# Optimization experiments

Hardware: AMD Instinct MI355X
Metric: run time of the kernel (lower is better)

## Reference

```python
import jax, jax.numpy as jnp
import numpy as np
from jax import lax

WEIGHT = 1.0
NUM_DILATION_STEPS = 20
FAR_DIST = 20.0


def _neighbor_count(x, kernel, num_classes):
    # grouped 3x3 conv with center tap zeroed, SAME padding (stride 1)
    return lax.conv_general_dilated(
        x, kernel, window_strides=(1, 1), padding='SAME',
        feature_group_count=num_classes,
        dimension_numbers=('NCHW', 'OIHW', 'NCHW'))


def fast_sdf(target_mask, num_classes):
    # target_mask: [B, H, W] int labels -> per-class chamfer-ish distance map [B, C, H, W]
    one_hot = jnp.transpose(jax.nn.one_hot(target_mask, num_classes, dtype=jnp.float32),
                            (0, 3, 1, 2))  # [B, C, H, W]
    foreground = (one_hot > 0.5).astype(jnp.float32)

    # 3x3 all-ones kernel with center zero, one per class (grouped conv)
    k = np.ones((num_classes, 1, 3, 3), dtype=np.float32)
    k[:, 0, 1, 1] = 0.0
    kernel = jnp.asarray(k)

    dist_map0 = jnp.zeros_like(foreground)

    def step(i, state):
        dist_map, current_mask = state
        dilated = (_neighbor_count(current_mask, kernel, num_classes) > 0).astype(jnp.float32)
        # note: faithful to torch code -- pixels with no neighbors vanish and
        # contribute negative increments, exactly as `dilated - current_mask` does
        new_pixels = dilated - current_mask
        dist_map = dist_map + new_pixels * (i + 1).astype(jnp.float32)
        return (dist_map, dilated)

    dist_map, current_mask = lax.fori_loop(0, NUM_DILATION_STEPS, step,
                                           (dist_map0, foreground))
    return jnp.where(current_mask == 0, FAR_DIST, dist_map)


def setup_inputs() -> dict:
    key = jax.random.key(0)
    k1, k2 = jax.random.split(key)
    B, C, H, W = 8, 19, 512, 512
    pred = jax.random.normal(k1, (B, C, H, W), dtype=jnp.float32)
    target = jax.random.randint(k2, (B, H, W), 0, C, dtype=jnp.int64)
    return {"pred": pred, "target": target}


def reference(pred, target):
    num_classes = pred.shape[1]
    probs = jax.nn.softmax(pred, axis=1)
    gt_sdf = lax.stop_gradient(fast_sdf(target, num_classes))
    loss = jnp.mean(probs * gt_sdf)
    return WEIGHT * loss
```

## Files before the change

kernel.cpp:

```cpp
#include <hip/hip_runtime.h>

#define B_ 8
#define C_ 19
#define H_ 512
#define W_ 512
#define HW_ (H_*W_)

#define HALO   20
#define INTR   8
#define WIN    48
#define NSTRIP 64

typedef unsigned long long u64;

__global__ __launch_bounds__(256) void mask_kernel(const int* __restrict__ target,
                                                   u64* __restrict__ masks) {
    __shared__ u64 mlds[64][21];
    const int blk  = blockIdx.x;
    const int b    = blk >> 6;
    const int base = (blk & 63) * 64;
    const int tid  = threadIdx.x;
    const int lane = tid & 63, wv = tid >> 6;
    const int* tgt = target + b * HW_;
    for (int t = 0; t < 16; ++t) {
        const int cl = wv * 16 + t;
        const int x  = tgt[(base + cl) * 64 + lane];
        u64 keep = 0;
        #pragma unroll
        for (int c = 0; c < C_; ++c) {
            u64 m = __ballot(x == c);
            if (lane == c) keep = m;
        }
        if (lane < C_) mlds[cl][lane] = keep;
    }
    __syncthreads();
    for (int idx = tid; idx < C_ * 64; idx += 256) {
        const int c = idx >> 6, wl = idx & 63;
        masks[((size_t)b * C_ + c) * 4096 + base + wl] = mlds[wl][c];
    }
}

__global__ __launch_bounds__(256, 2) void fused_kernel(const u64* __restrict__ masks,
                                                       const float* __restrict__ pred,
                                                       float* __restrict__ out) {
    __shared__ unsigned char sdfl[C_ * INTR * W_];
    __shared__ float part[4];
    const int blk   = blockIdx.x;
    const int strip = blk & 63;
    const int b     = blk >> 6;
    const int tid   = threadIdx.x;
    const int wv    = tid >> 6, lane = tid & 63;
    const int w     = lane & 7, g = lane >> 3;
    const int gytop = strip * INTR - HALO;

    for (int c = wv; c < C_; c += 4) {
        const u64* mk = masks + ((size_t)b * C_ + c) * 4096;
        u64 cov[6], h[6], iso[6], pl[6][5];

        #pragma unroll
        for (int i = 0; i < 6; ++i) {
            const int gy = gytop + g * 6 + i;
            cov[i] = (gy >= 0 && gy < H_) ? mk[gy * 8 + w] : 0;
            iso[i] = 0;
            #pragma unroll
            for (int j = 0; j < 5; ++j) pl[i][j] = 0;
        }

        u64 nc[6];
        {
            unsigned mp = 0, lp = 0;
            #pragma unroll
            for (int i = 0; i < 6; ++i) {
                mp |= (unsigned)(cov[i] >> 63) << i;
                lp |= ((unsigned)cov[i] & 1) << i;
            }
            unsigned fl = __shfl_up(mp, 1);   if (w == 0) fl = 0;
            unsigned fr = __shfl_down(lp, 1); if (w == 7) fr = 0;
            #pragma unroll
            for (int i = 0; i < 6; ++i) {
                nc[i] = (cov[i] << 1) | (cov[i] >> 1) | (u64)((fl >> i) & 1) | ((u64)((fr >> i) & 1) << 63);
                h[i]  = nc[i] | cov[i];
            }
        }

        bool active;
        {
            u64 hup = __shfl_up(h[5], 8);   if (g == 0) hup = 0;
            u64 hdn = __shfl_down(h[0], 8); if (g == 7) hdn = 0;
            u64 d[6], diffw = 0;
            #pragma unroll
            for (int i = 0; i < 6; ++i) {
                const u64 up  = (i > 0) ? h[i - 1] : hup;
                const u64 dn  = (i < 5) ? h[i + 1] : hdn;
                const u64 nbr = nc[i] | up | dn;
                iso[i] = cov[i] & ~nbr;
                const u64 nb = nbr & ~cov[i];
                pl[i][0] = nb;
                d[i] = cov[i] | nbr;
                diffw |= nb;
                cov[i] = d[i];
            }
            unsigned mp = 0, lp = 0;
            #pragma unroll
            for (int i = 0; i < 6; ++i) {
                mp |= (unsigned)(cov[i] >> 63) << i;
                lp |= ((unsigned)cov[i] & 1) << i;
            }
            unsigned fl = __shfl_up(mp, 1);   if (w == 0) fl = 0;
            unsigned fr = __shfl_down(lp, 1); if (w == 7) fr = 0;
            #pragma unroll
            for (int i = 0; i < 6; ++i)
                h[i] = cov[i] | (cov[i] << 1) | (cov[i] >> 1) | (u64)((fl >> i) & 1) | ((u64)((fr >> i) & 1) << 63);
            active = __any(diffw != 0);
        }

        if (active) {
            #pragma unroll
            for (int s = 2; s <= 19; ++s) {
                u64 hup = __shfl_up(h[5], 8);   if (g == 0) hup = 0;
                u64 hdn = __shfl_down(h[0], 8); if (g == 7) hdn = 0;
                u64 diffw = 0;
                #pragma unroll
                for (int i = 0; i < 6; ++i) {
                    const u64 up = (i > 0) ? h[i - 1] : hup;
                    const u64 dn = (i < 5) ? h[i + 1] : hdn;
                    const u64 d  = up | h[i] | dn;
                    const u64 nb = d ^ cov[i];
                    diffw |= nb;
                    if (s & 1)  pl[i][0] |= nb;
                    if (s & 2)  pl[i][1] |= nb;
                    if (s & 4)  pl[i][2] |= nb;
                    if (s & 8)  pl[i][3] |= nb;
                    if (s & 16) pl[i][4] |= nb;
                    cov[i] = d;
                }
                if (!__any(diffw != 0)) break;
                if (s < 19) {
                    unsigned mp = 0, lp = 0;
                    #pragma unroll
                    for (int i = 0; i < 6; ++i) {
                        mp |= (unsigned)(cov[i] >> 63) << i;
                        lp |= ((unsigned)cov[i] & 1) << i;
                    }
                    unsigned fl = __shfl_up(mp, 1);   if (w == 0) fl = 0;
                    unsigned fr = __shfl_down(lp, 1); if (w == 7) fr = 0;
                    #pragma unroll
                    for (int i = 0; i < 6; ++i)
                        h[i] = cov[i] | (cov[i] << 1) | (cov[i] >> 1) | (u64)((fl >> i) & 1) | ((u64)((fr >> i) & 1) << 63);
                }
            }
        }

        #pragma unroll
        for (int i = 0; i < 6; ++i) {
            const int lr = g * 6 + i;
            if (lr < HALO || lr >= HALO + INTR) continue;
            pl[i][0] |= iso[i];
            const u64 m = ~cov[i];
            pl[i][2] |= m;
            pl[i][4] |= m;
            u64* dst = (u64*)&sdfl[(c * INTR + (lr - HALO)) * W_ + w * 64];
            #pragma unroll
            for (int g2 = 0; g2 < 8; ++g2) {
                u64 x = 0;
                #pragma unroll
                for (int j = 0; j < 5; ++j)
                    x |= ((pl[i][j] >> (8 * g2)) & 0xFFULL) << (8 * j);
                u64 t;
                t = (x ^ (x >> 7))  & 0x00AA00AA00AA00AAULL; x ^= t ^ (t << 7);
                t = (x ^ (x >> 14)) & 0x0000CCCC0000CCCCULL; x ^= t ^ (t << 14);
                t = (x ^ (x >> 28)) & 0x00000000F0F0F0F0ULL; x ^= t ^ (t << 28);
                dst[g2] = x;
            }
        }
    }
    __syncthreads();

    float acc = 0.f;
    const float* pb = pred + (size_t)b * C_ * HW_ + (size_t)strip * INTR * W_;
    #pragma unroll
    for (int k = 0; k < 4; ++k) {
        const int p = k * 1024 + tid * 4;
        float4 den = {0.f, 0.f, 0.f, 0.f};
        float4 num = {0.f, 0.f, 0.f, 0.f};
        #pragma unroll
        for (int c = 0; c < C_; ++c) {
            const float4 v  = *(const float4*)(pb + (size_t)c * HW_ + p);
            const uchar4 sv = *(const uchar4*)&sdfl[c * 4096 + p];
            const float e0 = __expf(v.x), e1 = __expf(v.y);
            const float e2 = __expf(v.z), e3 = __expf(v.w);
            den.x += e0; den.y += e1; den.z += e2; den.w += e3;
            num.x = fmaf(e0, (float)sv.x, num.x);
            num.y = fmaf(e1, (float)sv.y, num.y);
            num.z = fmaf(e2, (float)sv.z, num.z);
            num.w = fmaf(e3, (float)sv.w, num.w);
        }
        acc += num.x / den.x + num.y / den.y + num.z / den.z + num.w / den.w;
    }

    #pragma unroll
    for (int off = 32; off > 0; off >>= 1) acc += __shfl_down(acc, off);
    if ((tid & 63) == 0) part[tid >> 6] = acc;
    __syncthreads();
    if (tid == 0) {
        float s = (part[0] + part[1]) + (part[2] + part[3]);
        atomicAdd(out, s * (1.0f / 39845888.0f));
    }
}

extern "C" void kernel_launch(void* const* d_in, const int* in_sizes, int n_in,
                              void* d_out, int out_size, void* d_ws, size_t ws_size,
                              hipStream_t stream) {
    const float* pred   = (const float*)d_in[0];
    const int*   target = (const int*)d_in[1];
    u64* masks = (u64*)d_ws;
    float* out = (float*)d_out;

    hipMemsetAsync(out, 0, sizeof(float), stream);
    mask_kernel<<<512, 256, 0, stream>>>(target, masks);
    fused_kernel<<<B_ * NSTRIP, 256, 0, stream>>>(masks, pred, out);
}
```

Baseline: 279.9 us.

## Split fused dilation+loss into separate dilate and loss kernels via workspace SDF

Splits the fused kernel in two. A dilate kernel runs one class per wave across five class-groups, which gives five times as many blocks and uses a much smaller LDS buffer, and writes a byte SDF map to global workspace. A separate streaming loss kernel then reads pred and the SDF to compute the softmax-weighted sum. This is meant to raise occupancy and parallelism, since the old fused kernel had only 512 blocks and used about 78KB of LDS. In exchange it adds about 40MB of global SDF writes and reads plus an extra launch, and the old path is kept as a fallback when the workspace is too small.

```diff
diff --git a/kernel.cpp b/kernel.cpp
--- a/kernel.cpp
+++ b/kernel.cpp
@@ -10,8 +10,12 @@
 #define INTR   8
 #define WIN    48
 #define NSTRIP 64
+#define CG_    5
 
 typedef unsigned long long u64;
+
+#define MASKS_BYTES 4980736ULL
+#define SDF_BYTES   39845888ULL
 
 __global__ __launch_bounds__(256) void mask_kernel(const int* __restrict__ target,
                                                    u64* __restrict__ masks) {
@@ -40,20 +44,21 @@
     }
 }
 
-__global__ __launch_bounds__(256, 2) void fused_kernel(const u64* __restrict__ masks,
-                                                       const float* __restrict__ pred,
-                                                       float* __restrict__ out) {
-    __shared__ unsigned char sdfl[C_ * INTR * W_];
-    __shared__ float part[4];
+__global__ __launch_bounds__(256) void dilate_kernel(const u64* __restrict__ masks,
+                                                     unsigned char* __restrict__ sdf) {
+    __shared__ unsigned char sdfl[4 * INTR * W_];
     const int blk   = blockIdx.x;
-    const int strip = blk & 63;
-    const int b     = blk >> 6;
+    const int cg    = blk % CG_;
+    const int rem   = blk / CG_;
+    const int strip = rem & 63;
+    const int b     = rem >> 6;
     const int tid   = threadIdx.x;
     const int wv    = tid >> 6, lane = tid & 63;
     const int w     = lane & 7, g = lane >> 3;
     const int gytop = strip * INTR - HALO;
-
-    for (int c = wv; c < C_; c += 4) {
+    const int c     = cg * 4 + wv;
+
+    if (c < C_) {
         const u64* mk = masks + ((size_t)b * C_ + c) * 4096;
         u64 cov[6], h[6], iso[6], pl[6][5];
 
@@ -159,7 +164,7 @@
             const u64 m = ~cov[i];
             pl[i][2] |= m;
             pl[i][4] |= m;
-            u64* dst = (u64*)&sdfl[(c * INTR + (lr - HALO)) * W_ + w * 64];
+            u64* dst = (u64*)&sdfl[(wv * INTR + (lr - HALO)) * W_ + w * 64];
             #pragma unroll
             for (int g2 = 0; g2 < 8; ++g2) {
                 u64 x = 0;
@@ -176,6 +181,187 @@
     }
     __syncthreads();
 
+    for (int idx = tid; idx < 4 * INTR * W_ / 16; idx += 256) {
+        const int cc = idx >> 8;
+        const int cl = cg * 4 + cc;
+        if (cl >= C_) continue;
+        const int off = (idx & 255) << 4;
+        *(uint4*)(sdf + ((size_t)b * C_ + cl) * HW_ + (size_t)strip * INTR * W_ + off) =
+            *(const uint4*)(&sdfl[cc * (INTR * W_) + off]);
+    }
+}
+
+__global__ __launch_bounds__(256) void loss_kernel(const float* __restrict__ pred,
+                                                   const unsigned char* __restrict__ sdf,
+                                                   float* __restrict__ out) {
+    __shared__ float part[4];
+    const int tid = threadIdx.x;
+    const size_t q = (size_t)blockIdx.x * 256 + tid;
+    const int b = (int)(q >> 16);
+    const int p = ((int)q & 65535) << 2;
+    const float* pb = pred + (size_t)b * C_ * HW_ + p;
+    const unsigned char* sb = sdf + (size_t)b * C_ * HW_ + p;
+    float4 den = {0.f, 0.f, 0.f, 0.f};
+    float4 num = {0.f, 0.f, 0.f, 0.f};
+    #pragma unroll
+    for (int c = 0; c < C_; ++c) {
+        const float4 v  = *(const float4*)(pb + (size_t)c * HW_);
+        const uchar4 sv = *(const uchar4*)(sb + (size_t)c * HW_);
+        const float e0 = __expf(v.x), e1 = __expf(v.y);
+        const float e2 = __expf(v.z), e3 = __expf(v.w);
+        den.x += e0; den.y += e1; den.z += e2; den.w += e3;
+        num.x = fmaf(e0, (float)sv.x, num.x);
+        num.y = fmaf(e1, (float)sv.y, num.y);
+        num.z = fmaf(e2, (float)sv.z, num.z);
+        num.w = fmaf(e3, (float)sv.w, num.w);
+    }
+    float acc = num.x / den.x + num.y / den.y + num.z / den.z + num.w / den.w;
+    #pragma unroll
+    for (int off = 32; off > 0; off >>= 1) acc += __shfl_down(acc, off);
+    if ((tid & 63) == 0) part[tid >> 6] = acc;
+    __syncthreads();
+    if (tid == 0) {
+        float s = (part[0] + part[1]) + (part[2] + part[3]);
+        atomicAdd(out, s * (1.0f / 39845888.0f));
+    }
+}
+
+__global__ __launch_bounds__(256, 2) void fused_kernel(const u64* __restrict__ masks,
+                                                       const float* __restrict__ pred,
+                                                       float* __restrict__ out) {
+    __shared__ unsigned char sdfl[C_ * INTR * W_];
+    __shared__ float part[4];
+    const int blk   = blockIdx.x;
+    const int strip = blk & 63;
+    const int b     = blk >> 6;
+    const int tid   = threadIdx.x;
+    const int wv    = tid >> 6, lane = tid & 63;
+    const int w     = lane & 7, g = lane >> 3;
+    const int gytop = strip * INTR - HALO;
+
+    for (int c = wv; c < C_; c += 4) {
+        const u64* mk = masks + ((size_t)b * C_ + c) * 4096;
+        u64 cov[6], h[6], iso[6], pl[6][5];
+
+        #pragma unroll
+        for (int i = 0; i < 6; ++i) {
+            const int gy = gytop + g * 6 + i;
+            cov[i] = (gy >= 0 && gy < H_) ? mk[gy * 8 + w] : 0;
+            iso[i] = 0;
+            #pragma unroll
+            for (int j = 0; j < 5; ++j) pl[i][j] = 0;
+        }
+
+        u64 nc[6];
+        {
+            unsigned mp = 0, lp = 0;
+            #pragma unroll
+            for (int i = 0; i < 6; ++i) {
+                mp |= (unsigned)(cov[i] >> 63) << i;
+                lp |= ((unsigned)cov[i] & 1) << i;
+            }
+            unsigned fl = __shfl_up(mp, 1);   if (w == 0) fl = 0;
+            unsigned fr = __shfl_down(lp, 1); if (w == 7) fr = 0;
+            #pragma unroll
+            for (int i = 0; i < 6; ++i) {
+                nc[i] = (cov[i] << 1) | (cov[i] >> 1) | (u64)((fl >> i) & 1) | ((u64)((fr >> i) & 1) << 63);
+                h[i]  = nc[i] | cov[i];
+            }
+        }
+
+        bool active;
+        {
+            u64 hup = __shfl_up(h[5], 8);   if (g == 0) hup = 0;
+            u64 hdn = __shfl_down(h[0], 8); if (g == 7) hdn = 0;
+            u64 d[6], diffw = 0;
+            #pragma unroll
+            for (int i = 0; i < 6; ++i) {
+                const u64 up  = (i > 0) ? h[i - 1] : hup;
+                const u64 dn  = (i < 5) ? h[i + 1] : hdn;
+                const u64 nbr = nc[i] | up | dn;
+                iso[i] = cov[i] & ~nbr;
+                const u64 nb = nbr & ~cov[i];
+                pl[i][0] = nb;
+                d[i] = cov[i] | nbr;
+                diffw |= nb;
+                cov[i] = d[i];
+            }
+            unsigned mp = 0, lp = 0;
+            #pragma unroll
+            for (int i = 0; i < 6; ++i) {
+                mp |= (unsigned)(cov[i] >> 63) << i;
+                lp |= ((unsigned)cov[i] & 1) << i;
+            }
+            unsigned fl = __shfl_up(mp, 1);   if (w == 0) fl = 0;
+            unsigned fr = __shfl_down(lp, 1); if (w == 7) fr = 0;
+            #pragma unroll
+            for (int i = 0; i < 6; ++i)
+                h[i] = cov[i] | (cov[i] << 1) | (cov[i] >> 1) | (u64)((fl >> i) & 1) | ((u64)((fr >> i) & 1) << 63);
+            active = __any(diffw != 0);
+        }
+
+        if (active) {
+            #pragma unroll
+            for (int s = 2; s <= 19; ++s) {
+                u64 hup = __shfl_up(h[5], 8);   if (g == 0) hup = 0;
+                u64 hdn = __shfl_down(h[0], 8); if (g == 7) hdn = 0;
+                u64 diffw = 0;
+                #pragma unroll
+                for (int i = 0; i < 6; ++i) {
+                    const u64 up = (i > 0) ? h[i - 1] : hup;
+                    const u64 dn = (i < 5) ? h[i + 1] : hdn;
+                    const u64 d  = up | h[i] | dn;
+                    const u64 nb = d ^ cov[i];
+                    diffw |= nb;
+                    if (s & 1)  pl[i][0] |= nb;
+                    if (s & 2)  pl[i][1] |= nb;
+                    if (s & 4)  pl[i][2] |= nb;
+                    if (s & 8)  pl[i][3] |= nb;
+                    if (s & 16) pl[i][4] |= nb;
+                    cov[i] = d;
+                }
+                if (!__any(diffw != 0)) break;
+                if (s < 19) {
+                    unsigned mp = 0, lp = 0;
+                    #pragma unroll
+                    for (int i = 0; i < 6; ++i) {
+                        mp |= (unsigned)(cov[i] >> 63) << i;
+                        lp |= ((unsigned)cov[i] & 1) << i;
+                    }
+                    unsigned fl = __shfl_up(mp, 1);   if (w == 0) fl = 0;
+                    unsigned fr = __shfl_down(lp, 1); if (w == 7) fr = 0;
+                    #pragma unroll
+                    for (int i = 0; i < 6; ++i)
+                        h[i] = cov[i] | (cov[i] << 1) | (cov[i] >> 1) | (u64)((fl >> i) & 1) | ((u64)((fr >> i) & 1) << 63);
+                }
+            }
+        }
+
+        #pragma unroll
+        for (int i = 0; i < 6; ++i) {
+            const int lr = g * 6 + i;
+            if (lr < HALO || lr >= HALO + INTR) continue;
+            pl[i][0] |= iso[i];
+            const u64 m = ~cov[i];
+            pl[i][2] |= m;
+            pl[i][4] |= m;
+            u64* dst = (u64*)&sdfl[(c * INTR + (lr - HALO)) * W_ + w * 64];
+            #pragma unroll
+            for (int g2 = 0; g2 < 8; ++g2) {
+                u64 x = 0;
+                #pragma unroll
+                for (int j = 0; j < 5; ++j)
+                    x |= ((pl[i][j] >> (8 * g2)) & 0xFFULL) << (8 * j);
+                u64 t;
+                t = (x ^ (x >> 7))  & 0x00AA00AA00AA00AAULL; x ^= t ^ (t << 7);
+                t = (x ^ (x >> 14)) & 0x0000CCCC0000CCCCULL; x ^= t ^ (t << 14);
+                t = (x ^ (x >> 28)) & 0x00000000F0F0F0F0ULL; x ^= t ^ (t << 28);
+                dst[g2] = x;
+            }
+        }
+    }
+    __syncthreads();
+
     float acc = 0.f;
     const float* pb = pred + (size_t)b * C_ * HW_ + (size_t)strip * INTR * W_;
     #pragma unroll
@@ -218,5 +404,12 @@
 
     hipMemsetAsync(out, 0, sizeof(float), stream);
     mask_kernel<<<512, 256, 0, stream>>>(target, masks);
-    fused_kernel<<<B_ * NSTRIP, 256, 0, stream>>>(masks, pred, out);
+
+    if (ws_size >= MASKS_BYTES + SDF_BYTES) {
+        unsigned char* sdf = (unsigned char*)d_ws + MASKS_BYTES;
+        dilate_kernel<<<B_ * NSTRIP * CG_, 256, 0, stream>>>(masks, sdf);
+        loss_kernel<<<(B_ * HW_ / 4) / 256, 256, 0, stream>>>(pred, sdf, out);
+    } else {
+        fused_kernel<<<B_ * NSTRIP, 256, 0, stream>>>(masks, pred, out);
+    }
 }
```

Measured after the change: 298.6 us. 1.07x slower.
